# Kernel tuning notes

Measured on AMD Instinct MI355X. Metric: run time of the kernel, lower is better.

The kernel has to match this reference:

```python
import jax, jax.numpy as jnp
import numpy as np

B, W, K = 8, 128, 2048          # batch, window_size, n_features(=n_nodes)
D = 2 * W                        # embed_dim after the *2 in __init__ (embed_dim=None -> window_size)

def setup_inputs() -> dict:
    key = jax.random.key(0)
    k1, k2, k3, k4 = jax.random.split(key, 4)
    x = jax.random.normal(k1, (B, W, K), dtype=jnp.float32)
    # nn.Linear(2W -> D), stored as [in, out] so y = cat @ W_lin + b_lin
    lim = 1.0 / np.sqrt(2 * W)
    W_lin = jax.random.uniform(k2, (2 * W, D), dtype=jnp.float32, minval=-lim, maxval=lim)
    b_lin = jax.random.uniform(k3, (D,), dtype=jnp.float32, minval=-lim, maxval=lim)
    # a: xavier_uniform with gain=1.414 on shape (D, 1)
    a_lim = 1.414 * np.sqrt(6.0 / (D + 1))
    a = jax.random.uniform(k4, (D, 1), dtype=jnp.float32, minval=-a_lim, maxval=a_lim)
    bias = jnp.zeros((K, K), dtype=jnp.float32)
    return {"x": x, "W_lin": W_lin, "b_lin": b_lin, "a": a, "bias": bias}

def reference(x, W_lin, b_lin, a, bias):
    # x: [B, W, K] -> v: [B, K, W]
    v = jnp.transpose(x, (0, 2, 1))
    av = a[:, 0]                                  # [D]
    # lin(cat(v_i, v_j)) @ a == (v_i @ W1) @ a + (v_j @ W2) @ a + b_lin @ a
    # This avoids the O(K^2 * 2W) pairwise tensor; math identical to the original.
    W1, W2 = W_lin[:W], W_lin[W:]                 # each [W, D]
    u1 = jnp.einsum('bkw,wd,d->bk', v, W1, av)    # [B, K] source-side score
    u2 = jnp.einsum('bkw,wd,d->bk', v, W2, av)    # [B, K] target-side score
    e = u1[:, :, None] + u2[:, None, :] + jnp.dot(b_lin, av) + bias  # [B, K, K]
    attention = jax.nn.softmax(e, axis=2)         # dropout p=0.0 (eval) -> identity
    h = jax.nn.sigmoid(jnp.matmul(attention, v))  # [B, K, W]
    return jnp.transpose(h, (0, 2, 1))            # [B, W, K]
```

## Files before the change

kernel.cpp:

```cpp
#include <hip/hip_runtime.h>
#include <hip/hip_bf16.h>

#define B_ 8
#define W_ 128
#define K_ 2048
#define D_ 256
#define WX 144
#define NC 256

typedef __attribute__((ext_vector_type(8))) short bf16x8;
typedef __attribute__((ext_vector_type(4))) float f32x4;
typedef unsigned int u32;

static __device__ __forceinline__ short f2bf(float f) {
    unsigned int u = __float_as_uint(f);
    unsigned int r = (u + 0x7FFFu + ((u >> 16) & 1u)) >> 16;
    return (short)r;
}

__global__ void k_w2v(const float* __restrict__ W_lin, const float* __restrict__ a,
                      float* __restrict__ w2v) {
    int w = blockIdx.x, l = threadIdx.x;
    float4 rv = ((const float4*)(W_lin + (size_t)(W_ + w) * D_))[l];
    float4 av = ((const float4*)a)[l];
    float acc = rv.x * av.x + rv.y * av.y + rv.z * av.z + rv.w * av.w;
    for (int m = 1; m < 64; m <<= 1) acc += __shfl_xor(acc, m);
    if (l == 0) w2v[w] = acc;
}

__global__ __launch_bounds__(512) void k_pe(const float* __restrict__ x,
        const float* __restrict__ w2v, const float* __restrict__ bias,
        short* __restrict__ xbt, short* __restrict__ e2t) {
    __shared__ float sc[696];
    int tid = threadIdx.x;
    int wid = tid >> 6;
    int lane = tid & 63;

    if (blockIdx.x < 512) {
        if (tid < W_) sc[tid] = w2v[tid];
        __syncthreads();
        int q = tid & 31, cw = tid >> 5;
        int bk0 = blockIdx.x * 32;
        int b = bk0 >> 11;
        int k = (bk0 & (K_ - 1)) + q;
        const float* xp = x + ((size_t)b * W_ + cw * 8) * K_ + k;
        float xv[8];
        float acc = 0.f;
#pragma unroll
        for (int w = 0; w < 8; ++w) {
            xv[w] = xp[(size_t)w * K_];
            acc += xv[w] * sc[cw * 8 + w];
        }
        sc[128 + cw * 33 + q] = acc;
        __syncthreads();
        if (tid < 32) {
            float s = 0.f;
#pragma unroll
            for (int cc = 0; cc < 16; ++cc) s += sc[128 + cc * 33 + tid];
            sc[656 + tid] = __expf(s);
        }
        __syncthreads();
        float e1q = sc[656 + q];
        short* xo = xbt + (((size_t)b * NC + (k >> 3)) * WX + cw * 8) * 8 + (k & 7);
#pragma unroll
        for (int w = 0; w < 8; ++w) xo[w * 8] = f2bf(xv[w] * e1q);
        if (tid < 32) {
            int kk = (bk0 & (K_ - 1)) + tid;
            xbt[(((size_t)b * NC + (kk >> 3)) * WX + 128) * 8 + (kk & 7)] = f2bf(sc[656 + tid]);
        }
        if (tid >= 64 && tid < 124) {
            int id = tid - 64;
            int cl = id / 15, wz = 129 + id % 15;
            int c = ((bk0 & (K_ - 1)) >> 3) + cl;
            bf16x8 z = {0, 0, 0, 0, 0, 0, 0, 0};
            *(bf16x8*)(xbt + (((size_t)b * NC + c) * WX + wz) * 8) = z;
        }
    } else {
        int i0e = (int)(blockIdx.x - 512) * 4;
        int il = tid & 3, cg = tid >> 2;
        const float4* brow = (const float4*)(bias + (size_t)(i0e + il) * K_);
        float4 v0 = brow[cg * 4 + 0];
        float4 v1 = brow[cg * 4 + 1];
        float4 v2 = brow[cg * 4 + 2];
        float4 v3 = brow[cg * 4 + 3];
        float m = fmaxf(fmaxf(fmaxf(v0.x, v0.y), fmaxf(v0.z, v0.w)),
                        fmaxf(fmaxf(v1.x, v1.y), fmaxf(v1.z, v1.w)));
        m = fmaxf(m, fmaxf(fmaxf(fmaxf(v2.x, v2.y), fmaxf(v2.z, v2.w)),
                           fmaxf(fmaxf(v3.x, v3.y), fmaxf(v3.z, v3.w))));
#pragma unroll
        for (int mm = 4; mm < 64; mm <<= 1) m = fmaxf(m, __shfl_xor(m, mm));
        if (lane < 4) sc[wid * 4 + lane] = m;
        __syncthreads();
        float mb = sc[il];
#pragma unroll
        for (int w = 1; w < 8; ++w) mb = fmaxf(mb, sc[w * 4 + il]);
        bf16x8 o0, o1;
        o0[0] = f2bf(__expf(v0.x - mb)); o0[1] = f2bf(__expf(v0.y - mb));
        o0[2] = f2bf(__expf(v0.z - mb)); o0[3] = f2bf(__expf(v0.w - mb));
        o0[4] = f2bf(__expf(v1.x - mb)); o0[5] = f2bf(__expf(v1.y - mb));
        o0[6] = f2bf(__expf(v1.z - mb)); o0[7] = f2bf(__expf(v1.w - mb));
        o1[0] = f2bf(__expf(v2.x - mb)); o1[1] = f2bf(__expf(v2.y - mb));
        o1[2] = f2bf(__expf(v2.z - mb)); o1[3] = f2bf(__expf(v2.w - mb));
        o1[4] = f2bf(__expf(v3.x - mb)); o1[5] = f2bf(__expf(v3.y - mb));
        o1[6] = f2bf(__expf(v3.z - mb)); o1[7] = f2bf(__expf(v3.w - mb));
        int i = i0e + il;
        *(bf16x8*)(e2t + ((size_t)(cg * 2) * K_ + i) * 8)     = o0;
        *(bf16x8*)(e2t + ((size_t)(cg * 2 + 1) * K_ + i) * 8) = o1;
    }
}

#define MF(a_, b_, c_) __builtin_amdgcn_mfma_f32_16x16x32_bf16(a_, b_, c_, 0, 0, 0)

#define GLLDS(gsrc, ldst) __builtin_amdgcn_global_load_lds(                      \
    (const u32 __attribute__((address_space(1)))*)(const void*)(gsrc),           \
    (u32 __attribute__((address_space(3)))*)(void*)(ldst), 16, 0, 0)

#define WAITV(n_) asm volatile("s_waitcnt vmcnt(" #n_ ")" ::: "memory")
#define BARR __builtin_amdgcn_s_barrier()

__global__ __launch_bounds__(512, 2) void k_gemm(const short* __restrict__ e2t,
        const short* __restrict__ xbt, float* __restrict__ out) {
    __shared__ __align__(16) char Bb[147456];
    int blk  = blockIdx.x;
    int b    = blk & 7;
    int i0   = (blk >> 3) * 64;
    int tid  = threadIdx.x;
    int wid  = tid >> 6;
    int lane = tid & 63;
    int il   = lane & 15;
    int kg   = lane >> 4;
    int mp   = wid & 1;
    int jq   = wid >> 1;

    int i0r = i0 + mp * 32;
    const short* eA = e2t + (((size_t)(jq * 64 + kg)) * K_ + i0r + il) * 8;
    size_t xbase = ((size_t)b * NC + jq * 64 + kg) * WX + il;
    char* jbuf = Bb + jq * 36864;

#define STG(s_) do {                                                             \
    const short* _g = xbt + (xbase + (size_t)(s_) * 4 * WX) * 8;                 \
    char* _d = jbuf + ((s_) & 3) * 9216;                                         \
    for (int f = mp; f < 9; f += 2)                                              \
        GLLDS(_g + f * 128, _d + f * 1024);                                      \
} while (0)

#define FAix(sl_, s_) do {                                                       \
    const short* _e = eA + (size_t)(s_) * 4 * K_ * 8;                            \
    ArA##sl_ = *(const bf16x8*)(_e);                                             \
    ArB##sl_ = *(const bf16x8*)(_e + 128);                                       \
} while (0)

    f32x4 qa0{0,0,0,0}, qa1{0,0,0,0}, qa2{0,0,0,0}, qa3{0,0,0,0}, qa4{0,0,0,0},
          qa5{0,0,0,0}, qa6{0,0,0,0}, qa7{0,0,0,0}, qa8{0,0,0,0};
    f32x4 qb0{0,0,0,0}, qb1{0,0,0,0}, qb2{0,0,0,0}, qb3{0,0,0,0}, qb4{0,0,0,0},
          qb5{0,0,0,0}, qb6{0,0,0,0}, qb7{0,0,0,0}, qb8{0,0,0,0};

#define CONS(s_, sl_) do {                                                       \
    const char* _bp = jbuf + ((s_) & 3) * 9216;                                  \
    bf16x8 b0 = *(const bf16x8*)(_bp +    0 + lane * 16);                        \
    bf16x8 b1 = *(const bf16x8*)(_bp + 1024 + lane * 16);                        \
    bf16x8 b2 = *(const bf16x8*)(_bp + 2048 + lane * 16);                        \
    bf16x8 b3 = *(const bf16x8*)(_bp + 3072 + lane * 16);                        \
    bf16x8 b4 = *(const bf16x8*)(_bp + 4096 + lane * 16);                        \
    bf16x8 b5 = *(const bf16x8*)(_bp + 5120 + lane * 16);                        \
    bf16x8 b6 = *(const bf16x8*)(_bp + 6144 + lane * 16);                        \
    bf16x8 b7 = *(const bf16x8*)(_bp + 7168 + lane * 16);                        \
    bf16x8 b8 = *(const bf16x8*)(_bp + 8192 + lane * 16);                        \
    __builtin_amdgcn_s_setprio(1);                                               \
    qa0 = MF(ArA##sl_, b0, qa0); qb0 = MF(ArB##sl_, b0, qb0);                    \
    qa1 = MF(ArA##sl_, b1, qa1); qb1 = MF(ArB##sl_, b1, qb1);                    \
    qa2 = MF(ArA##sl_, b2, qa2); qb2 = MF(ArB##sl_, b2, qb2);                    \
    qa3 = MF(ArA##sl_, b3, qa3); qb3 = MF(ArB##sl_, b3, qb3);                    \
    qa4 = MF(ArA##sl_, b4, qa4); qb4 = MF(ArB##sl_, b4, qb4);                    \
    qa5 = MF(ArA##sl_, b5, qa5); qb5 = MF(ArB##sl_, b5, qb5);                    \
    qa6 = MF(ArA##sl_, b6, qa6); qb6 = MF(ArB##sl_, b6, qb6);                    \
    qa7 = MF(ArA##sl_, b7, qa7); qb7 = MF(ArB##sl_, b7, qb7);                    \
    qa8 = MF(ArA##sl_, b8, qa8); qb8 = MF(ArB##sl_, b8, qb8);                    \
    __builtin_amdgcn_s_setprio(0);                                               \
} while (0)

#define STEP(s_, sl_, s2_, sl2_) do {                                            \
    FAix(sl2_, s2_); STG(s2_);                                                   \
    if (mp == 0) WAITV(14); else WAITV(12);                                      \
    BARR;                                                                        \
    CONS(s_, sl_);                                                               \
} while (0)

    bf16x8 ArA0, ArA1, ArA2, ArA3, ArB0, ArB1, ArB2, ArB3;
    FAix(0, 0); STG(0);
    FAix(1, 1); STG(1);

    STEP(0, 0, 2, 2);   STEP(1, 1, 3, 3);
    STEP(2, 2, 4, 0);   STEP(3, 3, 5, 1);
    STEP(4, 0, 6, 2);   STEP(5, 1, 7, 3);
    STEP(6, 2, 8, 0);   STEP(7, 3, 9, 1);
    STEP(8, 0, 10, 2);  STEP(9, 1, 11, 3);
    STEP(10, 2, 12, 0); STEP(11, 3, 13, 1);
    STEP(12, 0, 14, 2); STEP(13, 1, 15, 3);
    if (mp == 0) WAITV(7); else WAITV(6);
    BARR;
    CONS(14, 2);
    WAITV(0);
    BARR;
    CONS(15, 3);

    __syncthreads();

    f32x4* R = (f32x4*)Bb;
#define DUMPQ(slot_) do {                                                        \
    f32x4* _r = R + (size_t)(slot_) * 18 * 64 + lane;                            \
    _r[0*64]=qa0; _r[1*64]=qa1; _r[2*64]=qa2; _r[3*64]=qa3; _r[4*64]=qa4;        \
    _r[5*64]=qa5; _r[6*64]=qa6; _r[7*64]=qa7; _r[8*64]=qa8;                      \
    _r[9*64]=qb0; _r[10*64]=qb1; _r[11*64]=qb2; _r[12*64]=qb3; _r[13*64]=qb4;    \
    _r[14*64]=qb5; _r[15*64]=qb6; _r[16*64]=qb7; _r[17*64]=qb8; } while (0)
#define GATHQ(slot_) do {                                                        \
    f32x4* _r = R + (size_t)(slot_) * 18 * 64 + lane;                            \
    qa0+=_r[0*64]; qa1+=_r[1*64]; qa2+=_r[2*64]; qa3+=_r[3*64]; qa4+=_r[4*64];   \
    qa5+=_r[5*64]; qa6+=_r[6*64]; qa7+=_r[7*64]; qa8+=_r[8*64];                  \
    qb0+=_r[9*64]; qb1+=_r[10*64]; qb2+=_r[11*64]; qb3+=_r[12*64];               \
    qb4+=_r[13*64]; qb5+=_r[14*64]; qb6+=_r[15*64]; qb7+=_r[16*64];              \
    qb8+=_r[17*64]; } while (0)

    if (jq >= 2) DUMPQ((jq - 2) + 2 * mp);
    __syncthreads();
    if (jq < 2) GATHQ(jq + 2 * mp);
    __syncthreads();
    if (jq == 1) DUMPQ(mp);
    __syncthreads();
    if (jq == 0) {
        GATHQ(mp);
        float lA0 = 1.f / __shfl(qa8[0], kg * 16);
        float lA1 = 1.f / __shfl(qa8[1], kg * 16);
        float lA2 = 1.f / __shfl(qa8[2], kg * 16);
        float lA3 = 1.f / __shfl(qa8[3], kg * 16);
        float lB0 = 1.f / __shfl(qb8[0], kg * 16);
        float lB1 = 1.f / __shfl(qb8[1], kg * 16);
        float lB2 = 1.f / __shfl(qb8[2], kg * 16);
        float lB3 = 1.f / __shfl(qb8[3], kg * 16);
        float* obA = out + (size_t)b * W_ * K_ + i0r + kg * 4;
        float* obB = obA + 16;
#define STQ(ob_, n_, q_, l0_, l1_, l2_, l3_) do {                                \
        float4 o;                                                                \
        o.x = 1.f / (1.f + __expf(-q_[0] * l0_));                                \
        o.y = 1.f / (1.f + __expf(-q_[1] * l1_));                                \
        o.z = 1.f / (1.f + __expf(-q_[2] * l2_));                                \
        o.w = 1.f / (1.f + __expf(-q_[3] * l3_));                                \
        *(float4*)(ob_ + (size_t)((n_) * 16 + il) * K_) = o; } while (0)
        STQ(obA, 0, qa0, lA0, lA1, lA2, lA3); STQ(obB, 0, qb0, lB0, lB1, lB2, lB3);
        STQ(obA, 1, qa1, lA0, lA1, lA2, lA3); STQ(obB, 1, qb1, lB0, lB1, lB2, lB3);
        STQ(obA, 2, qa2, lA0, lA1, lA2, lA3); STQ(obB, 2, qb2, lB0, lB1, lB2, lB3);
        STQ(obA, 3, qa3, lA0, lA1, lA2, lA3); STQ(obB, 3, qb3, lB0, lB1, lB2, lB3);
        STQ(obA, 4, qa4, lA0, lA1, lA2, lA3); STQ(obB, 4, qb4, lB0, lB1, lB2, lB3);
        STQ(obA, 5, qa5, lA0, lA1, lA2, lA3); STQ(obB, 5, qb5, lB0, lB1, lB2, lB3);
        STQ(obA, 6, qa6, lA0, lA1, lA2, lA3); STQ(obB, 6, qb6, lB0, lB1, lB2, lB3);
        STQ(obA, 7, qa7, lA0, lA1, lA2, lA3); STQ(obB, 7, qb7, lB0, lB1, lB2, lB3);
#undef STQ
    }
}

extern "C" void kernel_launch(void* const* d_in, const int* in_sizes, int n_in,
                              void* d_out, int out_size, void* d_ws, size_t ws_size,
                              hipStream_t stream) {
    const float* x     = (const float*)d_in[0];
    const float* W_lin = (const float*)d_in[1];
    const float* a     = (const float*)d_in[3];
    const float* bias  = (const float*)d_in[4];
    float* out = (float*)d_out;

    float* w2v = (float*)d_ws;
    short* xbt = (short*)(w2v + 128);
    short* e2t = xbt + (size_t)B_ * NC * WX * 8;

    k_w2v <<<128, 64, 0, stream>>>(W_lin, a, w2v);
    k_pe  <<<1024, 512, 0, stream>>>(x, w2v, bias, xbt, e2t);
    k_gemm<<<256, 512, 0, stream>>>(e2t, xbt, out);
}
```

Measured before the change: 36.62 us.

## Double GEMM block to 1024 threads with 8-way K split and LDS-staged xbt writes

The GEMM kernel now runs 16 waves per block, splitting the reduction dimension eight ways instead of four. It drops from a 4-deep to a 2-deep LDS ring with a barrier after each consume step, interleaves LDS B-loads with MFMAs, and adds an extra reduction round across waves. Separately, the preprocessing kernel transposes its bf16 output through shared memory so xbt is written as 16-byte vectors instead of scattered 2-byte stores. The aim is more latency hiding and better write coalescing, at the cost of shallower prefetch, more barriers and a longer cross-wave reduction.

After: 65.43 us. 1.79x slower.

```diff
diff --git a/kernel.cpp b/kernel.cpp
--- a/kernel.cpp
+++ b/kernel.cpp
@@ -32,6 +32,7 @@
         const float* __restrict__ w2v, const float* __restrict__ bias,
         short* __restrict__ xbt, short* __restrict__ e2t) {
     __shared__ float sc[696];
+    __shared__ __align__(16) short ldt[128][4][8];
     int tid = threadIdx.x;
     int wid = tid >> 6;
     int lane = tid & 63;
@@ -43,6 +44,7 @@
         int bk0 = blockIdx.x * 32;
         int b = bk0 >> 11;
         int k = (bk0 & (K_ - 1)) + q;
+        int c0 = (bk0 & (K_ - 1)) >> 3;
         const float* xp = x + ((size_t)b * W_ + cw * 8) * K_ + k;
         float xv[8];
         float acc = 0.f;
@@ -61,9 +63,9 @@
         }
         __syncthreads();
         float e1q = sc[656 + q];
-        short* xo = xbt + (((size_t)b * NC + (k >> 3)) * WX + cw * 8) * 8 + (k & 7);
-#pragma unroll
-        for (int w = 0; w < 8; ++w) xo[w * 8] = f2bf(xv[w] * e1q);
+#pragma unroll
+        for (int w = 0; w < 8; ++w)
+            ldt[cw * 8 + w][q >> 3][q & 7] = f2bf(xv[w] * e1q);
         if (tid < 32) {
             int kk = (bk0 & (K_ - 1)) + tid;
             xbt[(((size_t)b * NC + (kk >> 3)) * WX + 128) * 8 + (kk & 7)] = f2bf(sc[656 + tid]);
@@ -71,9 +73,15 @@
         if (tid >= 64 && tid < 124) {
             int id = tid - 64;
             int cl = id / 15, wz = 129 + id % 15;
-            int c = ((bk0 & (K_ - 1)) >> 3) + cl;
+            int c = c0 + cl;
             bf16x8 z = {0, 0, 0, 0, 0, 0, 0, 0};
             *(bf16x8*)(xbt + (((size_t)b * NC + c) * WX + wz) * 8) = z;
+        }
+        __syncthreads();
+        {
+            int c = tid & 3, w = tid >> 2;
+            bf16x8 v = *(const bf16x8*)&ldt[w][c][0];
+            *(bf16x8*)(xbt + (((size_t)b * NC + c0 + c) * WX + w) * 8) = v;
         }
     } else {
         int i0e = (int)(blockIdx.x - 512) * 4;
@@ -118,7 +126,7 @@
 #define WAITV(n_) asm volatile("s_waitcnt vmcnt(" #n_ ")" ::: "memory")
 #define BARR __builtin_amdgcn_s_barrier()
 
-__global__ __launch_bounds__(512, 2) void k_gemm(const short* __restrict__ e2t,
+__global__ __launch_bounds__(1024, 4) void k_gemm(const short* __restrict__ e2t,
         const short* __restrict__ xbt, float* __restrict__ out) {
     __shared__ __align__(16) char Bb[147456];
     int blk  = blockIdx.x;
@@ -133,13 +141,13 @@
     int jq   = wid >> 1;
 
     int i0r = i0 + mp * 32;
-    const short* eA = e2t + (((size_t)(jq * 64 + kg)) * K_ + i0r + il) * 8;
-    size_t xbase = ((size_t)b * NC + jq * 64 + kg) * WX + il;
-    char* jbuf = Bb + jq * 36864;
+    const short* eA = e2t + (((size_t)(jq * 32 + kg)) * K_ + i0r + il) * 8;
+    size_t xbase = ((size_t)b * NC + jq * 32 + kg) * WX + il;
+    char* jbuf = Bb + jq * 18432;
 
 #define STG(s_) do {                                                             \
     const short* _g = xbt + (xbase + (size_t)(s_) * 4 * WX) * 8;                 \
-    char* _d = jbuf + ((s_) & 3) * 9216;                                         \
+    char* _d = jbuf + ((s_) & 1) * 9216;                                         \
     for (int f = mp; f < 9; f += 2)                                              \
         GLLDS(_g + f * 128, _d + f * 1024);                                      \
 } while (0)
@@ -156,23 +164,23 @@
           qb5{0,0,0,0}, qb6{0,0,0,0}, qb7{0,0,0,0}, qb8{0,0,0,0};
 
 #define CONS(s_, sl_) do {                                                       \
-    const char* _bp = jbuf + ((s_) & 3) * 9216;                                  \
+    const char* _bp = jbuf + ((s_) & 1) * 9216;                                  \
+    __builtin_amdgcn_s_setprio(1);                                               \
     bf16x8 b0 = *(const bf16x8*)(_bp +    0 + lane * 16);                        \
     bf16x8 b1 = *(const bf16x8*)(_bp + 1024 + lane * 16);                        \
     bf16x8 b2 = *(const bf16x8*)(_bp + 2048 + lane * 16);                        \
+    qa0 = MF(ArA##sl_, b0, qa0); qb0 = MF(ArB##sl_, b0, qb0);                    \
+    qa1 = MF(ArA##sl_, b1, qa1); qb1 = MF(ArB##sl_, b1, qb1);                    \
+    qa2 = MF(ArA##sl_, b2, qa2); qb2 = MF(ArB##sl_, b2, qb2);                    \
     bf16x8 b3 = *(const bf16x8*)(_bp + 3072 + lane * 16);                        \
     bf16x8 b4 = *(const bf16x8*)(_bp + 4096 + lane * 16);                        \
     bf16x8 b5 = *(const bf16x8*)(_bp + 5120 + lane * 16);                        \
+    qa3 = MF(ArA##sl_, b3, qa3); qb3 = MF(ArB##sl_, b3, qb3);                    \
+    qa4 = MF(ArA##sl_, b4, qa4); qb4 = MF(ArB##sl_, b4, qb4);                    \
+    qa5 = MF(ArA##sl_, b5, qa5); qb5 = MF(ArB##sl_, b5, qb5);                    \
     bf16x8 b6 = *(const bf16x8*)(_bp + 6144 + lane * 16);                        \
     bf16x8 b7 = *(const bf16x8*)(_bp + 7168 + lane * 16);                        \
     bf16x8 b8 = *(const bf16x8*)(_bp + 8192 + lane * 16);                        \
-    __builtin_amdgcn_s_setprio(1);                                               \
-    qa0 = MF(ArA##sl_, b0, qa0); qb0 = MF(ArB##sl_, b0, qb0);                    \
-    qa1 = MF(ArA##sl_, b1, qa1); qb1 = MF(ArB##sl_, b1, qb1);                    \
-    qa2 = MF(ArA##sl_, b2, qa2); qb2 = MF(ArB##sl_, b2, qb2);                    \
-    qa3 = MF(ArA##sl_, b3, qa3); qb3 = MF(ArB##sl_, b3, qb3);                    \
-    qa4 = MF(ArA##sl_, b4, qa4); qb4 = MF(ArB##sl_, b4, qb4);                    \
-    qa5 = MF(ArA##sl_, b5, qa5); qb5 = MF(ArB##sl_, b5, qb5);                    \
     qa6 = MF(ArA##sl_, b6, qa6); qb6 = MF(ArB##sl_, b6, qb6);                    \
     qa7 = MF(ArA##sl_, b7, qa7); qb7 = MF(ArB##sl_, b7, qb7);                    \
     qa8 = MF(ArA##sl_, b8, qa8); qb8 = MF(ArB##sl_, b8, qb8);                    \
@@ -180,29 +188,26 @@
 } while (0)
 
 #define STEP(s_, sl_, s2_, sl2_) do {                                            \
-    FAix(sl2_, s2_); STG(s2_);                                                   \
-    if (mp == 0) WAITV(14); else WAITV(12);                                      \
+    if (mp == 0) WAITV(7); else WAITV(6);                                        \
     BARR;                                                                        \
     CONS(s_, sl_);                                                               \
-} while (0)
-
-    bf16x8 ArA0, ArA1, ArA2, ArA3, ArB0, ArB1, ArB2, ArB3;
+    BARR;                                                                        \
+    FAix(sl2_, s2_); STG(s2_);                                                   \
+} while (0)
+
+    bf16x8 ArA0, ArB0, ArA1, ArB1;
     FAix(0, 0); STG(0);
     FAix(1, 1); STG(1);
 
-    STEP(0, 0, 2, 2);   STEP(1, 1, 3, 3);
-    STEP(2, 2, 4, 0);   STEP(3, 3, 5, 1);
-    STEP(4, 0, 6, 2);   STEP(5, 1, 7, 3);
-    STEP(6, 2, 8, 0);   STEP(7, 3, 9, 1);
-    STEP(8, 0, 10, 2);  STEP(9, 1, 11, 3);
-    STEP(10, 2, 12, 0); STEP(11, 3, 13, 1);
-    STEP(12, 0, 14, 2); STEP(13, 1, 15, 3);
+    STEP(0, 0, 2, 0); STEP(1, 1, 3, 1);
+    STEP(2, 0, 4, 0); STEP(3, 1, 5, 1);
+    STEP(4, 0, 6, 0); STEP(5, 1, 7, 1);
     if (mp == 0) WAITV(7); else WAITV(6);
     BARR;
-    CONS(14, 2);
+    CONS(6, 0);
     WAITV(0);
     BARR;
-    CONS(15, 3);
+    CONS(7, 1);
 
     __syncthreads();
 
@@ -221,14 +226,18 @@
     qb4+=_r[13*64]; qb5+=_r[14*64]; qb6+=_r[15*64]; qb7+=_r[16*64];              \
     qb8+=_r[17*64]; } while (0)
 
-    if (jq >= 2) DUMPQ((jq - 2) + 2 * mp);
-    __syncthreads();
-    if (jq < 2) GATHQ(jq + 2 * mp);
-    __syncthreads();
-    if (jq == 1) DUMPQ(mp);
+    if (jq >= 4) DUMPQ(mp * 4 + (jq - 4));
+    __syncthreads();
+    if (jq < 4) GATHQ(mp * 4 + jq);
+    __syncthreads();
+    if (jq == 2 || jq == 3) DUMPQ(mp * 4 + (jq - 2));
+    __syncthreads();
+    if (jq < 2) GATHQ(mp * 4 + jq);
+    __syncthreads();
+    if (jq == 1) DUMPQ(mp * 4);
     __syncthreads();
     if (jq == 0) {
-        GATHQ(mp);
+        GATHQ(mp * 4);
         float lA0 = 1.f / __shfl(qa8[0], kg * 16);
         float lA1 = 1.f / __shfl(qa8[1], kg * 16);
         float lA2 = 1.f / __shfl(qa8[2], kg * 16);
@@ -273,5 +282,5 @@
 
     k_w2v <<<128, 64, 0, stream>>>(W_lin, a, w2v);
     k_pe  <<<1024, 512, 0, stream>>>(x, w2v, bias, xbt, e2t);
-    k_gemm<<<256, 512, 0, stream>>>(e2t, xbt, out);
-}
+    k_gemm<<<256, 1024, 0, stream>>>(e2t, xbt, out);
+}
```
